# Kernel optimization log

Hardware: AMD Instinct MI355X
Metric: run time of the kernel (lower is better)

The kernel has to match this reference:

```python
import jax, jax.numpy as jnp
import numpy as np

N_NODES = 50000
N_EDGES = 800000
IN_DIM = 256
HID = 256
OUT = 2


def setup_inputs() -> dict:
    key = jax.random.key(0)
    ks = jax.random.split(key, 12)
    x = jax.random.normal(ks[0], (N_NODES, IN_DIM), dtype=jnp.float32)
    edge_index = jax.random.randint(ks[1], (2, N_EDGES), 0, N_NODES, dtype=jnp.int64)
    s = lambda fan_in: 1.0 / np.sqrt(fan_in)
    return {
        "x": x,
        "edge_index": edge_index,
        # SAGEConv 1: lin_l (neighbors, with bias), lin_r (root, no bias)
        "W1l": jax.random.normal(ks[2], (IN_DIM, HID), dtype=jnp.float32) * s(IN_DIM),
        "b1l": jnp.zeros((HID,), dtype=jnp.float32),
        "W1r": jax.random.normal(ks[3], (IN_DIM, HID), dtype=jnp.float32) * s(IN_DIM),
        # SAGEConv 2
        "W2l": jax.random.normal(ks[4], (HID, HID), dtype=jnp.float32) * s(HID),
        "b2l": jnp.zeros((HID,), dtype=jnp.float32),
        "W2r": jax.random.normal(ks[5], (HID, HID), dtype=jnp.float32) * s(HID),
        # edge MLP: Linear(2H -> H), ReLU, Linear(H -> OUT)
        "Wm1": jax.random.normal(ks[6], (2 * HID, HID), dtype=jnp.float32) * s(2 * HID),
        "bm1": jnp.zeros((HID,), dtype=jnp.float32),
        "Wm2": jax.random.normal(ks[7], (HID, OUT), dtype=jnp.float32) * s(HID),
        "bm2": jnp.zeros((OUT,), dtype=jnp.float32),
    }


def _sage_conv(x, src, dst, Wl, bl, Wr):
    # mean-aggregate source features at destination nodes (PyG SAGEConv, aggr='mean')
    n = x.shape[0]
    msg_sum = jax.ops.segment_sum(x[src], dst, num_segments=n)      # [N, D]
    deg = jax.ops.segment_sum(jnp.ones((src.shape[0],), x.dtype), dst, num_segments=n)
    agg = msg_sum / jnp.maximum(deg, 1.0)[:, None]
    return agg @ Wl + bl + x @ Wr


def reference(x, edge_index, W1l, b1l, W1r, W2l, b2l, W2r, Wm1, bm1, Wm2, bm2):
    src, dst = edge_index[0], edge_index[1]
    h = jax.nn.relu(_sage_conv(x, src, dst, W1l, b1l, W1r))
    h = jax.nn.relu(_sage_conv(h, src, dst, W2l, b2l, W2r))
    edge_reps = jnp.concatenate([h[src], h[dst]], axis=1)           # [E, 2H]
    hidden = jax.nn.relu(edge_reps @ Wm1 + bm1)
    logits = hidden @ Wm2 + bm2                                     # [E, OUT]
    return logits
```

## Files before the change

### kernel.cpp

```cpp
#include <hip/hip_runtime.h>

#define IN_DIM 256
#define HID 256
#define SCAN_CHUNK 512
#define PADW 264

typedef unsigned short ushort_t;
typedef __attribute__((ext_vector_type(8))) short short8;
typedef __attribute__((ext_vector_type(4))) float floatx4;

__device__ __forceinline__ float b2f(ushort_t h) {
    union { unsigned int u; float f; } c; c.u = ((unsigned int)h) << 16; return c.f;
}
__device__ __forceinline__ ushort_t f2b(float f) {
    union { float f; unsigned int u; } c; c.f = f;
    unsigned int u = c.u;
    unsigned int r = (u + 0x7fffu + ((u >> 16) & 1u)) >> 16;
    return (ushort_t)r;
}

__global__ void k_count_deg(const int* __restrict__ dst, int* __restrict__ deg, int E) {
    int e = blockIdx.x * blockDim.x + threadIdx.x;
    if (e < E) atomicAdd(&deg[dst[e]], 1);
}

__global__ __launch_bounds__(64) void k_chunk_sum(const int* __restrict__ deg,
                                                  int* __restrict__ partials, int N) {
    int lane = threadIdx.x;
    int base = blockIdx.x * SCAN_CHUNK + lane * 8;
    int s = 0;
#pragma unroll
    for (int i = 0; i < 8; ++i) s += (base + i < N) ? deg[base + i] : 0;
#pragma unroll
    for (int off = 32; off > 0; off >>= 1) s += __shfl_down(s, off, 64);
    if (lane == 0) partials[blockIdx.x] = s;
}

__global__ __launch_bounds__(64) void k_scan_partials(int* __restrict__ partials, int nb) {
    int lane = threadIdx.x;
    int run = 0;
    for (int base = 0; base < nb; base += 64) {
        int v = (base + lane < nb) ? partials[base + lane] : 0;
        int s = v;
#pragma unroll
        for (int off = 1; off < 64; off <<= 1) {
            int t = __shfl_up(s, off, 64);
            if (lane >= off) s += t;
        }
        if (base + lane < nb) partials[base + lane] = run + s - v;
        run += __shfl(s, 63, 64);
    }
}

__global__ __launch_bounds__(64) void k_scan_chunks(const int* __restrict__ deg,
                                                    const int* __restrict__ partials,
                                                    int* __restrict__ row_start,
                                                    int* __restrict__ cursor, int N) {
    int lane = threadIdx.x;
    int base = blockIdx.x * SCAN_CHUNK + lane * 8;
    int v[8]; int lsum = 0;
#pragma unroll
    for (int i = 0; i < 8; ++i) { v[i] = (base + i < N) ? deg[base + i] : 0; lsum += v[i]; }
    int pre = lsum;
#pragma unroll
    for (int off = 1; off < 64; off <<= 1) {
        int t = __shfl_up(pre, off, 64);
        if (lane >= off) pre += t;
    }
    pre -= lsum;
    int run = partials[blockIdx.x] + pre;
#pragma unroll
    for (int i = 0; i < 8; ++i) {
        if (base + i < N) { row_start[base + i] = run; cursor[base + i] = run; }
        run += v[i];
    }
}

__global__ void k_bucket(const int* __restrict__ src, const int* __restrict__ dst,
                         int* __restrict__ cursor, int2* __restrict__ csr, int E) {
    int e = blockIdx.x * blockDim.x + threadIdx.x;
    if (e < E) {
        int pos = atomicAdd(&cursor[dst[e]], 1);
        csr[pos] = make_int2(src[e], e);
    }
}

__global__ __launch_bounds__(256) void k_cast(const float* __restrict__ x,
                                              ushort_t* __restrict__ xb, int n4) {
    int i = blockIdx.x * blockDim.x + threadIdx.x;
    if (i >= n4) return;
    float4 v = ((const float4*)x)[i];
    ushort4 o;
    o.x = f2b(v.x); o.y = f2b(v.y); o.z = f2b(v.z); o.w = f2b(v.w);
    ((ushort4*)xb)[i] = o;
}

__global__ __launch_bounds__(64) void k_wprep6(const float* __restrict__ W1l, ushort_t* WF1l,
                                               const float* __restrict__ W1r, ushort_t* WF1r,
                                               const float* __restrict__ W2l, ushort_t* WF2l,
                                               const float* __restrict__ W2r, ushort_t* WF2r,
                                               const float* __restrict__ Wm1, ushort_t* WFm) {
    int m = blockIdx.x >> 7;
    int bb = blockIdx.x & 127;
    const float* Wsrc; ushort_t* WF; int nbTot, nb0;
    if (m == 0)      { Wsrc = W1l; WF = WF1l; nbTot = 16; nb0 = 0; }
    else if (m == 1) { Wsrc = W1r; WF = WF1r; nbTot = 16; nb0 = 0; }
    else if (m == 2) { Wsrc = W2l; WF = WF2l; nbTot = 16; nb0 = 0; }
    else if (m == 3) { Wsrc = W2r; WF = WF2r; nbTot = 16; nb0 = 0; }
    else if (m == 4) { Wsrc = Wm1; WF = WFm;  nbTot = 32; nb0 = 0; }
    else             { Wsrc = Wm1 + (size_t)256 * 256; WF = WFm; nbTot = 32; nb0 = 16; }
    int lane = threadIdx.x;
    int kb = bb >> 4, nbL = bb & 15;
    int k = kb * 32 + (lane >> 4) * 8;
    int n = nbL * 16 + (lane & 15);
    size_t dstb = (size_t)(kb * nbTot + nb0 + nbL) * 512 + lane * 8;
#pragma unroll
    for (int j = 0; j < 8; ++j) {
        WF[dstb + j] = f2b(Wsrc[(size_t)(k + j) * 256 + n]);
    }
}

__global__ __launch_bounds__(512, 4) void k_conv(const ushort_t* __restrict__ X,
                                                 const int2* __restrict__ csr,
                                                 const int* __restrict__ row_start,
                                                 const int* __restrict__ deg,
                                                 const ushort_t* __restrict__ WFl,
                                                 const ushort_t* __restrict__ WFr,
                                                 const float* __restrict__ bias,
                                                 int M,
                                                 ushort_t* __restrict__ C) {
    __shared__ ushort_t As[2][64 * PADW];
    const int tid = threadIdx.x;
    const int lane = tid & 63;
    const int w = tid >> 6;
    const int quad = lane >> 4, l16 = lane & 15;
    const int m0 = blockIdx.x * 64;

    for (int t = 0; t < 8; ++t) {
        int node = m0 + w * 8 + t;
        if (node >= M) continue;
        int start = row_start[node];
        int cnt = deg[node];
        const int2* sp = csr + start;
        float acc[16] = {};
        for (int b = 0; b < cnt; b += 64) {
            int nb = min(64, cnt - b);
            int sidx = (lane < nb) ? sp[b + lane].x : 0;

            int jA = (quad < nb) ? quad : 0;
            int jB = (4 + quad < nb) ? 4 + quad : 0;
            int sA = __shfl(sidx, jA, 64);
            int sB = __shfl(sidx, jB, 64);
            const ushort_t* rA = X + (size_t)sA * HID + l16 * 16;
            const ushort_t* rB = X + (size_t)sB * HID + l16 * 16;
            short8 a0 = *(const short8*)(rA);
            short8 a1 = *(const short8*)(rA + 8);
            short8 b0 = *(const short8*)(rB);
            short8 b1 = *(const short8*)(rB + 8);

            for (int j8 = 0; j8 < nb; j8 += 8) {
                bool vA = (j8 + quad) < nb, vB = (j8 + 4 + quad) < nb;
                short8 na0 = a0, na1 = a1, nb0 = b0, nb1 = b1;
                int j1 = j8 + 8;
                if (j1 < nb) {
                    int cA = (j1 + quad < nb) ? j1 + quad : 0;
                    int cB = (j1 + 4 + quad < nb) ? j1 + 4 + quad : 0;
                    int zA = __shfl(sidx, cA, 64);
                    int zB = __shfl(sidx, cB, 64);
                    const ushort_t* qA = X + (size_t)zA * HID + l16 * 16;
                    const ushort_t* qB = X + (size_t)zB * HID + l16 * 16;
                    na0 = *(const short8*)(qA);
                    na1 = *(const short8*)(qA + 8);
                    nb0 = *(const short8*)(qB);
                    nb1 = *(const short8*)(qB + 8);
                }
                if (vA) {
#pragma unroll
                    for (int i = 0; i < 8; ++i) {
                        acc[i]     += b2f((ushort_t)a0[i]);
                        acc[8 + i] += b2f((ushort_t)a1[i]);
                    }
                }
                if (vB) {
#pragma unroll
                    for (int i = 0; i < 8; ++i) {
                        acc[i]     += b2f((ushort_t)b0[i]);
                        acc[8 + i] += b2f((ushort_t)b1[i]);
                    }
                }
                a0 = na0; a1 = na1; b0 = nb0; b1 = nb1;
            }
        }
#pragma unroll
        for (int i = 0; i < 16; ++i) {
            acc[i] += __shfl_down(acc[i], 32, 64);
            acc[i] += __shfl_down(acc[i], 16, 64);
        }
        if (quad == 0) {
            float sc = 1.0f / (float)max(cnt, 1);
            short8 o0, o1;
#pragma unroll
            for (int i = 0; i < 8; ++i) {
                o0[i] = (short)f2b(acc[i] * sc);
                o1[i] = (short)f2b(acc[8 + i] * sc);
            }
            ushort_t* op = &As[0][(w * 8 + t) * PADW + l16 * 16];
            *(short8*)(op) = o0;
            *(short8*)(op + 8) = o1;
        }
    }

#pragma unroll
    for (int i = 0; i < 4; ++i) {
        int c = i * 512 + tid;
        int row = c >> 5, col = c & 31;
        int arow = m0 + row; if (arow >= M) arow = M - 1;
        *(uint4*)&As[1][row * PADW + col * 8] =
            *(const uint4*)(X + (size_t)arow * 256 + col * 8);
    }
    __syncthreads();

    const int wm = w >> 2, wn = w & 3;
    floatx4 acc[2][4] = {};
#pragma unroll
    for (int op = 0; op < 2; ++op) {
        const ushort_t* Ap = As[op];
        const ushort_t* WF = op ? WFr : WFl;
        const ushort_t* a0p = &Ap[(wm * 32 + l16) * PADW + quad * 8];
        const ushort_t* a1p = a0p + 16 * PADW;
        const ushort_t* wp = WF + (size_t)(wn * 4) * 512 + lane * 8;
#pragma unroll
        for (int kb = 0; kb < 8; ++kb) {
            short8 a0 = *(const short8*)(a0p + kb * 32);
            short8 a1 = *(const short8*)(a1p + kb * 32);
            const ushort_t* wkb = wp + (size_t)kb * 16 * 512;
#pragma unroll
            for (int nj = 0; nj < 4; ++nj) {
                short8 bj = *(const short8*)(wkb + nj * 512);
                acc[0][nj] = __builtin_amdgcn_mfma_f32_16x16x32_bf16(a0, bj, acc[0][nj], 0, 0, 0);
                acc[1][nj] = __builtin_amdgcn_mfma_f32_16x16x32_bf16(a1, bj, acc[1][nj], 0, 0, 0);
            }
        }
    }

#pragma unroll
    for (int mi = 0; mi < 2; ++mi) {
#pragma unroll
        for (int nj = 0; nj < 4; ++nj) {
            int col = wn * 64 + nj * 16 + l16;
            float b = bias[col];
            int rbase = m0 + wm * 32 + mi * 16 + quad * 4;
#pragma unroll
            for (int reg = 0; reg < 4; ++reg) {
                int r = rbase + reg;
                if (r >= M) continue;
                float v = fmaxf(acc[mi][nj][reg] + b, 0.f);
                C[(size_t)r * 256 + col] = f2b(v);
            }
        }
    }
}

__global__ __launch_bounds__(512) void k_mfma(const ushort_t* __restrict__ A1,
                                              const ushort_t* __restrict__ WF1,
                                              const float* __restrict__ bias, int relu,
                                              int M, int nbTot,
                                              ushort_t* __restrict__ C,
                                              ushort_t* __restrict__ C2) {
    __shared__ ushort_t As[64 * PADW];
    const int tid = threadIdx.x;
    const int lane = tid & 63;
    const int w = tid >> 6;
    const int wm = w >> 2, wn = w & 3;
    const int quad = lane >> 4, l16 = lane & 15;
    const int m0 = blockIdx.y * 64;
    const int n0 = blockIdx.x * 256;
    const int nbBase = (n0 >> 4) + wn * 4;

    floatx4 acc[2][4] = {};

#pragma unroll
    for (int i = 0; i < 4; ++i) {
        int c = i * 512 + tid;
        int row = c >> 5, col = c & 31;
        int arow = m0 + row; if (arow >= M) arow = M - 1;
        *(uint4*)&As[row * PADW + col * 8] =
            *(const uint4*)(A1 + (size_t)arow * 256 + col * 8);
    }
    __syncthreads();

    const ushort_t* a0p = &As[(wm * 32 + l16) * PADW + quad * 8];
    const ushort_t* a1p = a0p + 16 * PADW;
    const ushort_t* wp = WF1 + (size_t)nbBase * 512 + lane * 8;
#pragma unroll
    for (int kb = 0; kb < 8; ++kb) {
        short8 a0 = *(const short8*)(a0p + kb * 32);
        short8 a1 = *(const short8*)(a1p + kb * 32);
        const ushort_t* wkb = wp + (size_t)kb * nbTot * 512;
#pragma unroll
        for (int nj = 0; nj < 4; ++nj) {
            short8 bj = *(const short8*)(wkb + nj * 512);
            acc[0][nj] = __builtin_amdgcn_mfma_f32_16x16x32_bf16(a0, bj, acc[0][nj], 0, 0, 0);
            acc[1][nj] = __builtin_amdgcn_mfma_f32_16x16x32_bf16(a1, bj, acc[1][nj], 0, 0, 0);
        }
    }

#pragma unroll
    for (int mi = 0; mi < 2; ++mi) {
#pragma unroll
        for (int nj = 0; nj < 4; ++nj) {
            int col = n0 + wn * 64 + nj * 16 + l16;
            float b = bias ? bias[col] : 0.f;
            int rbase = m0 + wm * 32 + mi * 16 + quad * 4;
            ushort_t* dstp = C;
            int c = col;
            if (C2 && col >= 256) { dstp = C2; c = col - 256; }
#pragma unroll
            for (int reg = 0; reg < 4; ++reg) {
                int r = rbase + reg;
                if (r >= M) continue;
                float v = acc[mi][nj][reg] + b;
                if (relu) v = fmaxf(v, 0.f);
                dstp[(size_t)r * 256 + c] = f2b(v);
            }
        }
    }
}

__global__ __launch_bounds__(256) void k_edge(const ushort_t* __restrict__ P,
                                              const ushort_t* __restrict__ Q,
                                              const int2* __restrict__ csr,
                                              const int* __restrict__ row_start,
                                              const int* __restrict__ deg,
                                              const float* __restrict__ bm1,
                                              const float* __restrict__ Wm2,
                                              const float* __restrict__ bm2,
                                              float* __restrict__ out, int N, int stride) {
    int lane = threadIdx.x & 63;
    int wid = blockIdx.x * 4 + (threadIdx.x >> 6);
    int half = lane >> 5, l32 = lane & 31;

    float w0[8], w1[8], bb[8];
    const float* bp = bm1 + l32 * 8;
    const float2* wp = (const float2*)Wm2 + l32 * 8;
#pragma unroll
    for (int i = 0; i < 8; ++i) {
        float2 wv = wp[i];
        w0[i] = wv.x; w1[i] = wv.y;
        bb[i] = bp[i];
    }
    float bo0 = bm2[0], bo1 = bm2[1];

    for (int node = wid; node < N; node += stride) {
        int start = row_start[node];
        int cnt = deg[node];
        if (cnt == 0) continue;

        short8 qv = *(const short8*)(Q + (size_t)node * HID + l32 * 8);
        float qb[8];
#pragma unroll
        for (int i = 0; i < 8; ++i) qb[i] = b2f((ushort_t)qv[i]) + bb[i];

        const int2* sp = csr + start;
        for (int b = 0; b < cnt; b += 64) {
            int nb = min(64, cnt - b);
            int2 se = (lane < nb) ? sp[b + lane] : make_int2(0, 0);

            int iA = (half < nb) ? half : 0;
            int iB = (2 + half < nb) ? 2 + half : 0;
            int iC = (4 + half < nb) ? 4 + half : 0;
            int iD = (6 + half < nb) ? 6 + half : 0;
            int sA = __shfl(se.x, iA, 64);
            int sB = __shfl(se.x, iB, 64);
            int sC = __shfl(se.x, iC, 64);
            int sD = __shfl(se.x, iD, 64);
            short8 pA = *(const short8*)(P + (size_t)sA * HID + l32 * 8);
            short8 pB = *(const short8*)(P + (size_t)sB * HID + l32 * 8);
            short8 pC = *(const short8*)(P + (size_t)sC * HID + l32 * 8);
            short8 pD = *(const short8*)(P + (size_t)sD * HID + l32 * 8);

            for (int j0 = 0; j0 < nb; j0 += 8) {
                bool vA = j0 + half < nb, vB = j0 + 2 + half < nb;
                bool vC = j0 + 4 + half < nb, vD = j0 + 6 + half < nb;

                int kA = iA, kB = iB, kC = iC, kD = iD;
                short8 nA = pA, nB = pB, nC = pC, nD = pD;
                int j1 = j0 + 8;
                if (j1 < nb) {
                    kA = (j1 + half < nb) ? j1 + half : 0;
                    kB = (j1 + 2 + half < nb) ? j1 + 2 + half : 0;
                    kC = (j1 + 4 + half < nb) ? j1 + 4 + half : 0;
                    kD = (j1 + 6 + half < nb) ? j1 + 6 + half : 0;
                    int zA = __shfl(se.x, kA, 64);
                    int zB = __shfl(se.x, kB, 64);
                    int zC = __shfl(se.x, kC, 64);
                    int zD = __shfl(se.x, kD, 64);
                    nA = *(const short8*)(P + (size_t)zA * HID + l32 * 8);
                    nB = *(const short8*)(P + (size_t)zB * HID + l32 * 8);
                    nC = *(const short8*)(P + (size_t)zC * HID + l32 * 8);
                    nD = *(const short8*)(P + (size_t)zD * HID + l32 * 8);
                }

                float aA0 = 0.f, aA1 = 0.f, aB0 = 0.f, aB1 = 0.f;
                float aC0 = 0.f, aC1 = 0.f, aD0 = 0.f, aD1 = 0.f;
#pragma unroll
                for (int i = 0; i < 8; ++i) {
                    float hA = fmaxf(b2f((ushort_t)pA[i]) + qb[i], 0.f);
                    float hB = fmaxf(b2f((ushort_t)pB[i]) + qb[i], 0.f);
                    float hC = fmaxf(b2f((ushort_t)pC[i]) + qb[i], 0.f);
                    float hD = fmaxf(b2f((ushort_t)pD[i]) + qb[i], 0.f);
                    aA0 += hA * w0[i]; aA1 += hA * w1[i];
                    aB0 += hB * w0[i]; aB1 += hB * w1[i];
                    aC0 += hC * w0[i]; aC1 += hC * w1[i];
                    aD0 += hD * w0[i]; aD1 += hD * w1[i];
                }
#pragma unroll
                for (int off = 16; off > 0; off >>= 1) {
                    aA0 += __shfl_down(aA0, off, 32);
                    aA1 += __shfl_down(aA1, off, 32);
                    aB0 += __shfl_down(aB0, off, 32);
                    aB1 += __shfl_down(aB1, off, 32);
                    aC0 += __shfl_down(aC0, off, 32);
                    aC1 += __shfl_down(aC1, off, 32);
                    aD0 += __shfl_down(aD0, off, 32);
                    aD1 += __shfl_down(aD1, off, 32);
                }
                int eA = __shfl(se.y, iA, 64);
                int eB = __shfl(se.y, iB, 64);
                int eC = __shfl(se.y, iC, 64);
                int eD = __shfl(se.y, iD, 64);
                if (l32 == 0) {
                    if (vA) { float2 o; o.x = aA0 + bo0; o.y = aA1 + bo1; ((float2*)out)[eA] = o; }
                    if (vB) { float2 o; o.x = aB0 + bo0; o.y = aB1 + bo1; ((float2*)out)[eB] = o; }
                    if (vC) { float2 o; o.x = aC0 + bo0; o.y = aC1 + bo1; ((float2*)out)[eC] = o; }
                    if (vD) { float2 o; o.x = aD0 + bo0; o.y = aD1 + bo1; ((float2*)out)[eD] = o; }
                }
                pA = nA; pB = nB; pC = nC; pD = nD;
                iA = kA; iB = kB; iC = kC; iD = kD;
            }
        }
    }
}

extern "C" void kernel_launch(void* const* d_in, const int* in_sizes, int n_in,
                              void* d_out, int out_size, void* d_ws, size_t ws_size,
                              hipStream_t stream) {
    const float* x   = (const float*)d_in[0];
    const int*   ei  = (const int*)d_in[1];
    const float* W1l = (const float*)d_in[2];
    const float* b1l = (const float*)d_in[3];
    const float* W1r = (const float*)d_in[4];
    const float* W2l = (const float*)d_in[5];
    const float* b2l = (const float*)d_in[6];
    const float* W2r = (const float*)d_in[7];
    const float* Wm1 = (const float*)d_in[8];
    const float* bm1 = (const float*)d_in[9];
    const float* Wm2 = (const float*)d_in[10];
    const float* bm2 = (const float*)d_in[11];

    const int N = in_sizes[0] / IN_DIM;
    const int E = in_sizes[1] / 2;
    const int* src = ei;
    const int* dst = ei + E;
    const int NB = (N + SCAN_CHUNK - 1) / SCAN_CHUNK;

    char* ws = (char*)d_ws;
    size_t off = 0;
    auto alloc = [&](size_t bytes) { void* p = ws + off; off = (off + bytes + 255) & ~(size_t)255; return p; };
    int* deg       = (int*)alloc((size_t)N * 4);
    int* row_start = (int*)alloc((size_t)N * 4);
    int* cursor    = (int*)alloc((size_t)N * 4);
    int* partials  = (int*)alloc((size_t)(NB + 1) * 4);
    int2* csr      = (int2*)alloc((size_t)E * 8);
    size_t matB = (size_t)N * HID * sizeof(ushort_t);
    ushort_t* xb   = (ushort_t*)alloc(matB);
    ushort_t* h1b  = (ushort_t*)alloc(matB);
    ushort_t* h2b  = (ushort_t*)alloc(matB);
    ushort_t* Pb   = (ushort_t*)alloc(matB);
    ushort_t* Qb   = (ushort_t*)alloc(matB);
    size_t wfB  = (size_t)8 * 16 * 512 * sizeof(ushort_t);
    ushort_t* WF1l = (ushort_t*)alloc(wfB);
    ushort_t* WF1r = (ushort_t*)alloc(wfB);
    ushort_t* WF2l = (ushort_t*)alloc(wfB);
    ushort_t* WF2r = (ushort_t*)alloc(wfB);
    ushort_t* WFm  = (ushort_t*)alloc(wfB * 2);
    float* out = (float*)d_out;

    int mrows = (N + 63) / 64;

    hipMemsetAsync(deg, 0, (size_t)N * 4, stream);
    k_count_deg<<<(E + 255) / 256, 256, 0, stream>>>(dst, deg, E);
    k_chunk_sum<<<NB, 64, 0, stream>>>(deg, partials, N);
    k_scan_partials<<<1, 64, 0, stream>>>(partials, NB);
    k_scan_chunks<<<NB, 64, 0, stream>>>(deg, partials, row_start, cursor, N);
    k_bucket<<<(E + 255) / 256, 256, 0, stream>>>(src, dst, cursor, csr, E);

    k_cast<<<(N * HID / 4 + 255) / 256, 256, 0, stream>>>(x, xb, N * HID / 4);
    k_wprep6<<<768, 64, 0, stream>>>(W1l, WF1l, W1r, WF1r, W2l, WF2l, W2r, WF2r, Wm1, WFm);

    k_conv<<<mrows, 512, 0, stream>>>(xb, csr, row_start, deg, WF1l, WF1r, b1l, N, h1b);

    k_conv<<<mrows, 512, 0, stream>>>(h1b, csr, row_start, deg, WF2l, WF2r, b2l, N, h2b);

    k_mfma<<<dim3(2, mrows), 512, 0, stream>>>(h2b, WFm, nullptr, 0, N, 32, Pb, Qb);

    const int EB = 2048;
    k_edge<<<EB, 256, 0, stream>>>(Pb, Qb, csr, row_start, deg, bm1, Wm2, bm2, out, N, EB * 4);
}
```

Before: 506.5 us.

## Fuse edge-MLP projection GEMM into second SAGE conv epilogue

The second conv kernel now writes its ReLU'd bf16 output tile into shared memory and immediately multiplies it by the packed edge-MLP first-layer weights, producing the P and Q projections directly. This removes the separate projection GEMM launch and the round trip of h2 through global memory. In exchange, the conv kernel does twice the MFMA work per block with 64 accumulator registers per lane, which may raise register pressure and reduce occupancy under the 4-blocks-per-CU launch bound.

```diff
diff --git a/kernel.cpp b/kernel.cpp
--- a/kernel.cpp
+++ b/kernel.cpp
@@ -120,6 +120,7 @@
     }
 }
 
+template<int FUSE>
 __global__ __launch_bounds__(512, 4) void k_conv(const ushort_t* __restrict__ X,
                                                  const int2* __restrict__ csr,
                                                  const int* __restrict__ row_start,
@@ -128,7 +129,10 @@
                                                  const ushort_t* __restrict__ WFr,
                                                  const float* __restrict__ bias,
                                                  int M,
-                                                 ushort_t* __restrict__ C) {
+                                                 ushort_t* __restrict__ C,
+                                                 const ushort_t* __restrict__ WFm2,
+                                                 ushort_t* __restrict__ Pout,
+                                                 ushort_t* __restrict__ Qout) {
     __shared__ ushort_t As[2][64 * PADW];
     const int tid = threadIdx.x;
     const int lane = tid & 63;
@@ -243,85 +247,72 @@
         }
     }
 
-#pragma unroll
-    for (int mi = 0; mi < 2; ++mi) {
-#pragma unroll
-        for (int nj = 0; nj < 4; ++nj) {
-            int col = wn * 64 + nj * 16 + l16;
-            float b = bias[col];
-            int rbase = m0 + wm * 32 + mi * 16 + quad * 4;
-#pragma unroll
-            for (int reg = 0; reg < 4; ++reg) {
-                int r = rbase + reg;
-                if (r >= M) continue;
-                float v = fmaxf(acc[mi][nj][reg] + b, 0.f);
-                C[(size_t)r * 256 + col] = f2b(v);
-            }
-        }
-    }
-}
-
-__global__ __launch_bounds__(512) void k_mfma(const ushort_t* __restrict__ A1,
-                                              const ushort_t* __restrict__ WF1,
-                                              const float* __restrict__ bias, int relu,
-                                              int M, int nbTot,
-                                              ushort_t* __restrict__ C,
-                                              ushort_t* __restrict__ C2) {
-    __shared__ ushort_t As[64 * PADW];
-    const int tid = threadIdx.x;
-    const int lane = tid & 63;
-    const int w = tid >> 6;
-    const int wm = w >> 2, wn = w & 3;
-    const int quad = lane >> 4, l16 = lane & 15;
-    const int m0 = blockIdx.y * 64;
-    const int n0 = blockIdx.x * 256;
-    const int nbBase = (n0 >> 4) + wn * 4;
-
-    floatx4 acc[2][4] = {};
-
-#pragma unroll
-    for (int i = 0; i < 4; ++i) {
-        int c = i * 512 + tid;
-        int row = c >> 5, col = c & 31;
-        int arow = m0 + row; if (arow >= M) arow = M - 1;
-        *(uint4*)&As[row * PADW + col * 8] =
-            *(const uint4*)(A1 + (size_t)arow * 256 + col * 8);
-    }
-    __syncthreads();
-
-    const ushort_t* a0p = &As[(wm * 32 + l16) * PADW + quad * 8];
-    const ushort_t* a1p = a0p + 16 * PADW;
-    const ushort_t* wp = WF1 + (size_t)nbBase * 512 + lane * 8;
-#pragma unroll
-    for (int kb = 0; kb < 8; ++kb) {
-        short8 a0 = *(const short8*)(a0p + kb * 32);
-        short8 a1 = *(const short8*)(a1p + kb * 32);
-        const ushort_t* wkb = wp + (size_t)kb * nbTot * 512;
-#pragma unroll
-        for (int nj = 0; nj < 4; ++nj) {
-            short8 bj = *(const short8*)(wkb + nj * 512);
-            acc[0][nj] = __builtin_amdgcn_mfma_f32_16x16x32_bf16(a0, bj, acc[0][nj], 0, 0, 0);
-            acc[1][nj] = __builtin_amdgcn_mfma_f32_16x16x32_bf16(a1, bj, acc[1][nj], 0, 0, 0);
-        }
-    }
-
-#pragma unroll
-    for (int mi = 0; mi < 2; ++mi) {
-#pragma unroll
-        for (int nj = 0; nj < 4; ++nj) {
-            int col = n0 + wn * 64 + nj * 16 + l16;
-            float b = bias ? bias[col] : 0.f;
-            int rbase = m0 + wm * 32 + mi * 16 + quad * 4;
-            ushort_t* dstp = C;
-            int c = col;
-            if (C2 && col >= 256) { dstp = C2; c = col - 256; }
-#pragma unroll
-            for (int reg = 0; reg < 4; ++reg) {
-                int r = rbase + reg;
-                if (r >= M) continue;
-                float v = acc[mi][nj][reg] + b;
-                if (relu) v = fmaxf(v, 0.f);
-                dstp[(size_t)r * 256 + c] = f2b(v);
+    if constexpr (FUSE == 0) {
+#pragma unroll
+        for (int mi = 0; mi < 2; ++mi) {
+#pragma unroll
+            for (int nj = 0; nj < 4; ++nj) {
+                int col = wn * 64 + nj * 16 + l16;
+                float b = bias[col];
+                int rbase = m0 + wm * 32 + mi * 16 + quad * 4;
+#pragma unroll
+                for (int reg = 0; reg < 4; ++reg) {
+                    int r = rbase + reg;
+                    if (r >= M) continue;
+                    float v = fmaxf(acc[mi][nj][reg] + b, 0.f);
+                    C[(size_t)r * 256 + col] = f2b(v);
+                }
+            }
+        }
+    } else {
+        __syncthreads();
+#pragma unroll
+        for (int mi = 0; mi < 2; ++mi) {
+#pragma unroll
+            for (int nj = 0; nj < 4; ++nj) {
+                int col = wn * 64 + nj * 16 + l16;
+                float b = bias[col];
+                int rloc = wm * 32 + mi * 16 + quad * 4;
+#pragma unroll
+                for (int reg = 0; reg < 4; ++reg) {
+                    float v = fmaxf(acc[mi][nj][reg] + b, 0.f);
+                    As[0][(rloc + reg) * PADW + col] = f2b(v);
+                }
+            }
+        }
+        __syncthreads();
+
+        floatx4 acc2[2][8] = {};
+        const ushort_t* a0p = &As[0][(wm * 32 + l16) * PADW + quad * 8];
+        const ushort_t* a1p = a0p + 16 * PADW;
+        const ushort_t* wp = WFm2 + (size_t)(wn * 8) * 512 + lane * 8;
+#pragma unroll
+        for (int kb = 0; kb < 8; ++kb) {
+            short8 a0 = *(const short8*)(a0p + kb * 32);
+            short8 a1 = *(const short8*)(a1p + kb * 32);
+            const ushort_t* wkb = wp + (size_t)kb * 32 * 512;
+#pragma unroll
+            for (int nj = 0; nj < 8; ++nj) {
+                short8 bj = *(const short8*)(wkb + nj * 512);
+                acc2[0][nj] = __builtin_amdgcn_mfma_f32_16x16x32_bf16(a0, bj, acc2[0][nj], 0, 0, 0);
+                acc2[1][nj] = __builtin_amdgcn_mfma_f32_16x16x32_bf16(a1, bj, acc2[1][nj], 0, 0, 0);
+            }
+        }
+
+#pragma unroll
+        for (int mi = 0; mi < 2; ++mi) {
+#pragma unroll
+            for (int nj = 0; nj < 8; ++nj) {
+                int col = wn * 128 + nj * 16 + l16;
+                ushort_t* dstp = (col < 256) ? Pout : Qout;
+                int c = col & 255;
+                int rbase = m0 + wm * 32 + mi * 16 + quad * 4;
+#pragma unroll
+                for (int reg = 0; reg < 4; ++reg) {
+                    int r = rbase + reg;
+                    if (r >= M) continue;
+                    dstp[(size_t)r * 256 + c] = f2b(acc2[mi][nj][reg]);
+                }
             }
         }
     }
@@ -475,7 +466,6 @@
     size_t matB = (size_t)N * HID * sizeof(ushort_t);
     ushort_t* xb   = (ushort_t*)alloc(matB);
     ushort_t* h1b  = (ushort_t*)alloc(matB);
-    ushort_t* h2b  = (ushort_t*)alloc(matB);
     ushort_t* Pb   = (ushort_t*)alloc(matB);
     ushort_t* Qb   = (ushort_t*)alloc(matB);
     size_t wfB  = (size_t)8 * 16 * 512 * sizeof(ushort_t);
@@ -498,11 +488,11 @@
     k_cast<<<(N * HID / 4 + 255) / 256, 256, 0, stream>>>(x, xb, N * HID / 4);
     k_wprep6<<<768, 64, 0, stream>>>(W1l, WF1l, W1r, WF1r, W2l, WF2l, W2r, WF2r, Wm1, WFm);
 
-    k_conv<<<mrows, 512, 0, stream>>>(xb, csr, row_start, deg, WF1l, WF1r, b1l, N, h1b);
-
-    k_conv<<<mrows, 512, 0, stream>>>(h1b, csr, row_start, deg, WF2l, WF2r, b2l, N, h2b);
-
-    k_mfma<<<dim3(2, mrows), 512, 0, stream>>>(h2b, WFm, nullptr, 0, N, 32, Pb, Qb);
+    k_conv<0><<<mrows, 512, 0, stream>>>(xb, csr, row_start, deg, WF1l, WF1r, b1l, N, h1b,
+                                         nullptr, nullptr, nullptr);
+
+    k_conv<1><<<mrows, 512, 0, stream>>>(h1b, csr, row_start, deg, WF2l, WF2r, b2l, N, nullptr,
+                                         WFm, Pb, Qb);
 
     const int EB = 2048;
     k_edge<<<EB, 256, 0, stream>>>(Pb, Qb, csr, row_start, deg, bm1, Wm2, bm2, out, N, EB * 4);
```

New measurement: 482.5 us. 4.7% less time.
